# Kernel tuning notes

Measured on AMD Instinct MI355X. Metric: run time of the kernel, lower is better.

Reference implementation:

```python
import jax, jax.numpy as jnp
import numpy as np
from jax.scipy.special import logsumexp

NEG = -1e9
B, L = 128, 256


def setup_inputs() -> dict:
    key = jax.random.key(0)
    s_span = jax.random.normal(key, (B, L, L), dtype=jnp.float32)
    # fencepost lengths: logZ read at s[b, 0, lens[b]]; use full-length sentences
    lens = jnp.full((B,), L - 1, dtype=jnp.int32)
    return {"s_span": s_span, "lens": lens}


def _diag_layout(s_span):
    """span_d[b, w, i] = s_span[b, i, i+w] (clipped; invalid cells masked by callers)."""
    Ls = s_span.shape[1]
    w = jnp.arange(Ls)[:, None]          # [L,1]
    i = jnp.arange(Ls)[None, :]          # [1,L]
    j = jnp.clip(i + w, 0, Ls - 1)       # [L,L]
    return s_span[:, i, j]               # [B,L,L]


def cyk_partition(s_span, lens):
    Bb, Ls = s_span.shape[:2]
    span_d = _diag_layout(s_span)                       # [B,L(width),L(start)]
    i = jnp.arange(Ls)
    k = jnp.arange(Ls)
    # init: width-1 spans
    s0 = jnp.full((Bb, Ls, Ls), NEG, dtype=s_span.dtype)
    s0 = s0.at[:, 1, :].set(jnp.where(i < Ls - 1, span_d[:, 1, :], NEG))

    def step(s_d, w):
        # left[b,k,i]  = s[b, i, i+k]        = s_d[b, k, i]
        # right[b,k,i] = s[b, i+k, i+w]      = s_d[b, w-k, i+k]
        rr = jnp.clip(w - k, 0, Ls - 1)                       # [L]
        cc = jnp.clip(i[None, :] + k[:, None], 0, Ls - 1)     # [L,L]
        right = s_d[:, rr[:, None], cc]                       # [B,L,L]
        split_mask = (k[:, None] >= 1) & (k[:, None] <= w - 1)
        scores = jnp.where(split_mask, s_d + right, NEG)      # [B,L(k),L(i)]
        composed = logsumexp(scores, axis=1)                  # [B,L(i)]
        composed = jnp.where(i < Ls - w, composed + span_d[:, w, :], NEG)
        s_d = s_d.at[:, w, :].set(composed)
        return s_d, None

    s_d, _ = jax.lax.scan(step, s0, jnp.arange(2, Ls))
    # logZ = s[b, 0, lens[b]] = s_d[b, lens[b], 0]
    return s_d[jnp.arange(Bb), lens, 0]


def reference(s_span, lens):
    return cyk_partition(s_span, lens)
```

## Files before the change

### kernel.cpp

```cpp
#include <hip/hip_runtime.h>

#define LL 256
#define NEGV -1000000000.0f
#define LOG2E 1.4426950408889634f
#define LN2 0.6931471805599453f

__device__ __forceinline__ int off_of(int w) {
    return (w << 8) - ((w * (w - 1)) >> 1);
}

#define SHIFT_OFF 32896
#define PART_OFF  33152
#define LDS_DWORDS 37248

template<int NC>
__device__ __forceinline__ void inner_loop(const float* chart, const float* shift,
                                           float* part, int w, int wave, int lane) {
    float s[NC];
    float sh[NC];
    #pragma unroll
    for (int q = 0; q < NC; ++q) { s[q] = 0.f; sh[q] = shift[lane + 64 * q]; }

    const int k0 = 1 + wave;
    if (k0 <= w - 1) {
        int aL = off_of(k0) + lane;
        int aR = off_of(w - k0) + k0 + lane;
        int dL = 3976 - 16 * k0;
        int dR = 16 * (w - k0) - 4216;
        for (int k = k0; k <= w - 1; k += 16) {
            #pragma unroll
            for (int q = 0; q < NC; ++q) {
                float l = chart[aL + 64 * q];
                float r = chart[aR + 64 * q];
                s[q] += __builtin_amdgcn_exp2f(l + r - sh[q]);
            }
            aL += dL; dL -= 256;
            aR += dR; dR -= 256;
        }
    }
    #pragma unroll
    for (int q = 0; q < NC; ++q) part[wave * 256 + lane + 64 * q] = s[q];
}

__global__ __launch_bounds__(1024, 1)
void cyk_kernel(const float* __restrict__ s, const int* __restrict__ lens,
                float* __restrict__ out) {
    extern __shared__ float lds[];
    float* chart = lds;
    float* shift = lds + SHIFT_OFF;
    float* part  = lds + PART_OFF;

    const int b    = blockIdx.x;
    const int tid  = threadIdx.x;
    const int wave = tid >> 6;
    const int lane = tid & 63;
    const float* sb = s + (size_t)b * (LL * LL);

    for (int i = tid; i < LL; i += 1024) chart[i] = NEGV * LOG2E;

    for (int idx = tid; idx < (LL * LL) / 4; idx += 1024) {
        float4 v = reinterpret_cast<const float4*>(sb)[idx];
        int r  = (idx * 4) >> 8;
        int c0 = (idx * 4) & (LL - 1);
        float vv[4] = {v.x, v.y, v.z, v.w};
        #pragma unroll
        for (int q = 0; q < 4; ++q) {
            int w = (c0 + q) - r;
            if (w > 0) chart[off_of(w) + r] = vv[q] * LOG2E;
        }
    }
    __syncthreads();

    if (tid < LL - 2) shift[tid] = chart[256 + tid] + chart[256 + tid + 1];
    __syncthreads();

    for (int w = 2; w < LL; ++w) {
        const int ncols = LL - w;
        const int nslots = (ncols + 63) >> 6;

        switch (nslots) {
            case 4: inner_loop<4>(chart, shift, part, w, wave, lane); break;
            case 3: inner_loop<3>(chart, shift, part, w, wave, lane); break;
            case 2: inner_loop<2>(chart, shift, part, w, wave, lane); break;
            default: inner_loop<1>(chart, shift, part, w, wave, lane); break;
        }
        __syncthreads();

        if (tid < ncols) {
            float tot = 0.f;
            #pragma unroll
            for (int t = 0; t < 16; ++t) tot += part[t * 256 + tid];
            float newv = chart[off_of(w) + tid] + shift[tid]
                       + __builtin_amdgcn_logf(tot);
            chart[off_of(w) + tid] = newv;

            float p1 = newv + chart[256 + tid + w];
            float p2 = p1;
            if (w >= 3) {
                int km = (w + 1) >> 1;
                p2 = chart[off_of(km) + tid] + chart[off_of(w + 1 - km) + tid + km];
            }
            shift[tid] = fmaxf(p1, p2);
        }
        __syncthreads();
    }

    if (tid == 0) {
        int len = lens[b];
        len = len < 0 ? 0 : (len > LL - 1 ? LL - 1 : len);
        out[b] = chart[off_of(len)] * LN2;
    }
}

extern "C" void kernel_launch(void* const* d_in, const int* in_sizes, int n_in,
                              void* d_out, int out_size, void* d_ws, size_t ws_size,
                              hipStream_t stream) {
    const float* s_span = (const float*)d_in[0];
    const int*   lens   = (const int*)d_in[1];
    float*       out    = (float*)d_out;
    const int B = in_sizes[1];
    const int lds_bytes = LDS_DWORDS * 4;

    (void)hipFuncSetAttribute((const void*)cyk_kernel,
                              hipFuncAttributeMaxDynamicSharedMemorySize,
                              lds_bytes);

    cyk_kernel<<<B, 1024, lds_bytes, stream>>>(s_span, lens, out);
}
```

Before: 412.7 us.

## Process CYK widths in groups of four, sharing left-operand loads across widths

Restructures the width recurrence to handle four consecutive widths per sweep. Each left chart value loaded once is reused for four right operands, and splits that depend on not-yet-finished widths are deferred to short per-width cleanup steps. Per-wave partials are now combined with LDS atomicAdds into a small buffer instead of a 16-way reduction array, and the shift is computed directly from a middle split. The aim is to cut LDS loads and the number of barrier-separated sweep phases per width, at the cost of more barriers in the cleanup steps and LDS atomic contention.

```diff
diff --git a/kernel.cpp b/kernel.cpp
--- a/kernel.cpp
+++ b/kernel.cpp
@@ -10,36 +10,89 @@
 }
 
 #define SHIFT_OFF 32896
-#define PART_OFF  33152
-#define LDS_DWORDS 37248
+#define PART_OFF  (32896 + 1024)
+#define LDS_DWORDS (32896 + 2048)
 
-template<int NC>
-__device__ __forceinline__ void inner_loop(const float* chart, const float* shift,
-                                           float* part, int w, int wave, int lane) {
-    float s[NC];
-    float sh[NC];
+template<int NC, int FG>
+__device__ __forceinline__ void sweep(const float* chart, const float* shift,
+                                      float* part, int wb, int wave, int lane) {
+    float sum[NC][FG];
+    float sh[NC][FG];
     #pragma unroll
-    for (int q = 0; q < NC; ++q) { s[q] = 0.f; sh[q] = shift[lane + 64 * q]; }
+    for (int q = 0; q < NC; ++q)
+        #pragma unroll
+        for (int j = 0; j < FG; ++j) {
+            sum[q][j] = 0.f;
+            sh[q][j] = shift[j * 256 + lane + 64 * q];
+        }
 
-    const int k0 = 1 + wave;
-    if (k0 <= w - 1) {
+    const int wbm1 = wb - 1;
+    const int k0 = FG + wave;
+    if (k0 <= wbm1) {
         int aL = off_of(k0) + lane;
-        int aR = off_of(w - k0) + k0 + lane;
+        int aR = off_of(wb - k0) + k0 + lane;
         int dL = 3976 - 16 * k0;
-        int dR = 16 * (w - k0) - 4216;
-        for (int k = k0; k <= w - 1; k += 16) {
+        int dR = 16 * (wb - k0) - 4216;
+        int e  = 256 - wb + k0;
+        for (int k = k0; k <= wbm1; k += 16) {
+            float lv[NC];
             #pragma unroll
-            for (int q = 0; q < NC; ++q) {
-                float l = chart[aL + 64 * q];
-                float r = chart[aR + 64 * q];
-                s[q] += __builtin_amdgcn_exp2f(l + r - sh[q]);
+            for (int q = 0; q < NC; ++q) lv[q] = chart[aL + 64 * q];
+            int aj = aR, ej = e;
+            #pragma unroll
+            for (int j = 0; j < FG; ++j) {
+                #pragma unroll
+                for (int q = 0; q < NC; ++q) {
+                    float r = chart[aj + 64 * q];
+                    sum[q][j] += __builtin_amdgcn_exp2f(lv[q] + r - sh[q][j]);
+                }
+                aj += ej; ej -= 1;
             }
             aL += dL; dL -= 256;
             aR += dR; dR -= 256;
+            e += 16;
+        }
+        #pragma unroll
+        for (int q = 0; q < NC; ++q)
+            #pragma unroll
+            for (int j = 0; j < FG; ++j)
+                atomicAdd(&part[j * 256 + lane + 64 * q], sum[q][j]);
+    }
+}
+
+template<int FG>
+__device__ __forceinline__ void prephase(const float* chart, float* shift,
+                                         float* part, int wb, int tid) {
+    if (tid < FG * 256) {
+        part[tid] = 0.f;
+        int col = tid & 255, j = tid >> 8;
+        int wp = wb + j;
+        if (col < LL - wp) {
+            int km = wp >> 1;
+            shift[tid] = chart[off_of(km) + col] + chart[off_of(wp - km) + col + km];
         }
     }
-    #pragma unroll
-    for (int q = 0; q < NC; ++q) part[wave * 256 + lane + 64 * q] = s[q];
+}
+
+template<int FG, int J>
+__device__ __forceinline__ void cleanup(float* chart, const float* shift,
+                                        const float* part, int wb, int tid) {
+    const int wp = wb + J;
+    if (tid < LL - wp) {
+        float shv = shift[J * 256 + tid];
+        float tot = part[J * 256 + tid];
+        #pragma unroll
+        for (int k = 1; k <= FG - 1; ++k)
+            tot += __builtin_amdgcn_exp2f(chart[off_of(k) + tid] +
+                     chart[off_of(wp - k) + tid + k] - shv);
+        #pragma unroll
+        for (int m = 0; m < J; ++m) {
+            int k = wb + m;
+            tot += __builtin_amdgcn_exp2f(chart[off_of(k) + tid] +
+                     chart[off_of(wp - k) + tid + k] - shv);
+        }
+        chart[off_of(wp) + tid] += shv + __builtin_amdgcn_logf(tot);
+    }
 }
 
 __global__ __launch_bounds__(1024, 1)
@@ -71,38 +124,43 @@
     }
     __syncthreads();
 
-    if (tid < LL - 2) shift[tid] = chart[256 + tid] + chart[256 + tid + 1];
-    __syncthreads();
-
-    for (int w = 2; w < LL; ++w) {
-        const int ncols = LL - w;
-        const int nslots = (ncols + 63) >> 6;
-
-        switch (nslots) {
-            case 4: inner_loop<4>(chart, shift, part, w, wave, lane); break;
-            case 3: inner_loop<3>(chart, shift, part, w, wave, lane); break;
-            case 2: inner_loop<2>(chart, shift, part, w, wave, lane); break;
-            default: inner_loop<1>(chart, shift, part, w, wave, lane); break;
+    for (int wp = 2; wp <= 5; ++wp) {
+        if (tid < LL - wp) {
+            float shv = chart[256 + tid] + chart[off_of(wp - 1) + tid + 1];
+            float tot = 0.f;
+            for (int k = 1; k <= wp - 1; ++k)
+                tot += __builtin_amdgcn_exp2f(chart[off_of(k) + tid] +
+                         chart[off_of(wp - k) + tid + k] - shv);
+            chart[off_of(wp) + tid] += shv + __builtin_amdgcn_logf(tot);
         }
         __syncthreads();
+    }
 
-        if (tid < ncols) {
-            float tot = 0.f;
-            #pragma unroll
-            for (int t = 0; t < 16; ++t) tot += part[t * 256 + tid];
-            float newv = chart[off_of(w) + tid] + shift[tid]
-                       + __builtin_amdgcn_logf(tot);
-            chart[off_of(w) + tid] = newv;
-
-            float p1 = newv + chart[256 + tid + w];
-            float p2 = p1;
-            if (w >= 3) {
-                int km = (w + 1) >> 1;
-                p2 = chart[off_of(km) + tid] + chart[off_of(w + 1 - km) + tid + km];
-            }
-            shift[tid] = fmaxf(p1, p2);
+    for (int wb = 6; wb <= 250; wb += 4) {
+        const int NC = (LL - wb + 63) >> 6;
+        prephase<4>(chart, shift, part, wb, tid);
+        __syncthreads();
+        switch (NC) {
+            case 4: sweep<4, 4>(chart, shift, part, wb, wave, lane); break;
+            case 3: sweep<3, 4>(chart, shift, part, wb, wave, lane); break;
+            case 2: sweep<2, 4>(chart, shift, part, wb, wave, lane); break;
+            default: sweep<1, 4>(chart, shift, part, wb, wave, lane); break;
         }
         __syncthreads();
+        cleanup<4, 0>(chart, shift, part, wb, tid); __syncthreads();
+        cleanup<4, 1>(chart, shift, part, wb, tid); __syncthreads();
+        cleanup<4, 2>(chart, shift, part, wb, tid); __syncthreads();
+        cleanup<4, 3>(chart, shift, part, wb, tid); __syncthreads();
+    }
+
+    {
+        const int wb = 254;
+        prephase<2>(chart, shift, part, wb, tid);
+        __syncthreads();
+        sweep<1, 2>(chart, shift, part, wb, wave, lane);
+        __syncthreads();
+        cleanup<2, 0>(chart, shift, part, wb, tid); __syncthreads();
+        cleanup<2, 1>(chart, shift, part, wb, tid); __syncthreads();
     }
 
     if (tid == 0) {
```

After: 1.055 ms. +155.6%, slower.

## Pad diagonal chart rows to 16B alignment and use contiguous per-lane column blocks

Applied to the files above, without the earlier changes.

Each diagonal row of the LDS chart is padded so every row starts on a 4-float boundary. Each lane now owns 4, 2 or 1 contiguous columns instead of columns strided by 64, so the left operand can be fetched with one aligned float4 LDS load. The unaligned right operand is still read with scalar loads. The aim is fewer LDS load instructions in the inner logsumexp sweep. In exchange, LDS use grows slightly and the wider per-lane access pattern may raise bank conflicts.

```diff
diff --git a/kernel.cpp b/kernel.cpp
--- a/kernel.cpp
+++ b/kernel.cpp
@@ -5,41 +5,84 @@
 #define LOG2E 1.4426950408889634f
 #define LN2 0.6931471805599453f
 
-__device__ __forceinline__ int off_of(int w) {
-    return (w << 8) - ((w * (w - 1)) >> 1);
+__device__ __forceinline__ int poff(int w) {
+    int t = w & 3;
+    return (w << 8) - ((w * (w - 1)) >> 1) + 6 * (w >> 2) + ((t * (t - 1)) >> 1);
 }
 
-#define SHIFT_OFF 32896
-#define PART_OFF  33152
-#define LDS_DWORDS 37248
+#define SHIFT_OFF 33280
+#define PART_OFF  33536
+#define LDS_DWORDS 37632
 
-template<int NC>
-__device__ __forceinline__ void inner_loop(const float* chart, const float* shift,
-                                           float* part, int w, int wave, int lane) {
-    float s[NC];
-    float sh[NC];
-    #pragma unroll
-    for (int q = 0; q < NC; ++q) { s[q] = 0.f; sh[q] = shift[lane + 64 * q]; }
 
+__device__ __forceinline__ void sweep4(const float* chart, const float* shift,
+                                       float* part, int w, int wave, int lane) {
+    const int c0 = 4 * lane;
+    float4 sh = *reinterpret_cast<const float4*>(&shift[c0]);
+    float4 s = {0.f, 0.f, 0.f, 0.f};
     const int k0 = 1 + wave;
     if (k0 <= w - 1) {
-        int aL = off_of(k0) + lane;
-        int aR = off_of(w - k0) + k0 + lane;
-        int dL = 3976 - 16 * k0;
-        int dR = 16 * (w - k0) - 4216;
+        const float4* chart4 = reinterpret_cast<const float4*>(chart);
+        int aL4 = (poff(k0) >> 2) + lane;
+        int aR  = poff(w - k0) + k0 + c0;
+        int dL  = 4000 - 16 * k0;
+        int dR  = 16 * (w - k0) - 4240;
         for (int k = k0; k <= w - 1; k += 16) {
-            #pragma unroll
-            for (int q = 0; q < NC; ++q) {
-                float l = chart[aL + 64 * q];
-                float r = chart[aR + 64 * q];
-                s[q] += __builtin_amdgcn_exp2f(l + r - sh[q]);
-            }
+            float4 lv = chart4[aL4];
+            float r0 = chart[aR], r1 = chart[aR + 1];
+            float r2 = chart[aR + 2], r3 = chart[aR + 3];
+            s.x += __builtin_amdgcn_exp2f(lv.x + r0 - sh.x);
+            s.y += __builtin_amdgcn_exp2f(lv.y + r1 - sh.y);
+            s.z += __builtin_amdgcn_exp2f(lv.z + r2 - sh.z);
+            s.w += __builtin_amdgcn_exp2f(lv.w + r3 - sh.w);
+            aL4 += (dL >> 2); dL -= 256;
+            aR  += dR;        dR -= 256;
+        }
+    }
+    *reinterpret_cast<float4*>(&part[wave * 256 + c0]) = s;
+}
+
+__device__ __forceinline__ void sweep2(const float* chart, const float* shift,
+                                       float* part, int w, int wave, int lane) {
+    const int c0 = 2 * lane;
+    float sh0 = shift[c0], sh1 = shift[c0 + 1];
+    float s0 = 0.f, s1 = 0.f;
+    const int k0 = 1 + wave;
+    if (k0 <= w - 1) {
+        int aL = poff(k0) + c0;
+        int aR = poff(w - k0) + k0 + c0;
+        int dL = 4000 - 16 * k0;
+        int dR = 16 * (w - k0) - 4240;
+        for (int k = k0; k <= w - 1; k += 16) {
+            float l0 = chart[aL], l1 = chart[aL + 1];
+            float r0 = chart[aR], r1 = chart[aR + 1];
+            s0 += __builtin_amdgcn_exp2f(l0 + r0 - sh0);
+            s1 += __builtin_amdgcn_exp2f(l1 + r1 - sh1);
             aL += dL; dL -= 256;
             aR += dR; dR -= 256;
         }
     }
-    #pragma unroll
-    for (int q = 0; q < NC; ++q) part[wave * 256 + lane + 64 * q] = s[q];
+    part[wave * 256 + c0]     = s0;
+    part[wave * 256 + c0 + 1] = s1;
+}
+
+__device__ __forceinline__ void sweep1(const float* chart, const float* shift,
+                                       float* part, int w, int wave, int lane) {
+    float sh0 = shift[lane];
+    float s0 = 0.f;
+    const int k0 = 1 + wave;
+    if (k0 <= w - 1) {
+        int aL = poff(k0) + lane;
+        int aR = poff(w - k0) + k0 + lane;
+        int dL = 4000 - 16 * k0;
+        int dR = 16 * (w - k0) - 4240;
+        for (int k = k0; k <= w - 1; k += 16) {
+            s0 += __builtin_amdgcn_exp2f(chart[aL] + chart[aR] - sh0);
+            aL += dL; dL -= 256;
+            aR += dR; dR -= 256;
+        }
+    }
+    part[wave * 256 + lane] = s0;
 }
 
 __global__ __launch_bounds__(1024, 1)
@@ -66,7 +109,7 @@
         #pragma unroll
         for (int q = 0; q < 4; ++q) {
             int w = (c0 + q) - r;
-            if (w > 0) chart[off_of(w) + r] = vv[q] * LOG2E;
+            if (w > 0) chart[poff(w) + r] = vv[q] * LOG2E;
         }
     }
     __syncthreads();
@@ -76,29 +119,25 @@
 
     for (int w = 2; w < LL; ++w) {
         const int ncols = LL - w;
-        const int nslots = (ncols + 63) >> 6;
 
-        switch (nslots) {
-            case 4: inner_loop<4>(chart, shift, part, w, wave, lane); break;
-            case 3: inner_loop<3>(chart, shift, part, w, wave, lane); break;
-            case 2: inner_loop<2>(chart, shift, part, w, wave, lane); break;
-            default: inner_loop<1>(chart, shift, part, w, wave, lane); break;
-        }
+        if (w < 128)      sweep4(chart, shift, part, w, wave, lane);
+        else if (w < 192) sweep2(chart, shift, part, w, wave, lane);
+        else              sweep1(chart, shift, part, w, wave, lane);
         __syncthreads();
 
         if (tid < ncols) {
             float tot = 0.f;
             #pragma unroll
             for (int t = 0; t < 16; ++t) tot += part[t * 256 + tid];
-            float newv = chart[off_of(w) + tid] + shift[tid]
+            float newv = chart[poff(w) + tid] + shift[tid]
                        + __builtin_amdgcn_logf(tot);
-            chart[off_of(w) + tid] = newv;
+            chart[poff(w) + tid] = newv;
 
             float p1 = newv + chart[256 + tid + w];
             float p2 = p1;
             if (w >= 3) {
                 int km = (w + 1) >> 1;
-                p2 = chart[off_of(km) + tid] + chart[off_of(w + 1 - km) + tid + km];
+                p2 = chart[poff(km) + tid] + chart[poff(w + 1 - km) + tid + km];
             }
             shift[tid] = fmaxf(p1, p2);
         }
@@ -108,7 +147,7 @@
     if (tid == 0) {
         int len = lens[b];
         len = len < 0 ? 0 : (len > LL - 1 ? LL - 1 : len);
-        out[b] = chart[off_of(len)] * LN2;
+        out[b] = chart[poff(len)] * LN2;
     }
 }
 
```

Measured after the change: 489.6 us. +18.6%, slower.
